# Optimization experiments

Hardware: AMD Instinct MI355X
Metric: run time of the kernel (lower is better)

## Reference

```python
import jax, jax.numpy as jnp
import numpy as np

MODEL_DIM = 1024
NUM_HEAD = 16
HEAD_DIM = MODEL_DIM // NUM_HEAD
B, S = 2, 2048


def setup_inputs() -> dict:
    key = jax.random.key(0)
    ks = jax.random.split(key, 13)
    s = 1.0 / np.sqrt(MODEL_DIM)
    inp = {
        "q": jax.random.normal(ks[0], (B, S, MODEL_DIM), jnp.float32),
        "k": jax.random.normal(ks[1], (B, S, MODEL_DIM), jnp.float32),
        "v": jax.random.normal(ks[2], (B, S, MODEL_DIM), jnp.float32),
        "mask": jax.random.randint(ks[3], (S, S), 0, 2, jnp.int32),
        "w_q": jax.random.normal(ks[4], (MODEL_DIM, MODEL_DIM), jnp.float32) * s,
        "b_q": jax.random.normal(ks[5], (MODEL_DIM,), jnp.float32) * s,
        "w_k": jax.random.normal(ks[6], (MODEL_DIM, MODEL_DIM), jnp.float32) * s,
        "b_k": jax.random.normal(ks[7], (MODEL_DIM,), jnp.float32) * s,
        "w_v": jax.random.normal(ks[8], (MODEL_DIM, MODEL_DIM), jnp.float32) * s,
        "b_v": jax.random.normal(ks[9], (MODEL_DIM,), jnp.float32) * s,
        "w_o": jax.random.normal(ks[10], (MODEL_DIM, MODEL_DIM), jnp.float32) * s,
        "b_o": jax.random.normal(ks[11], (MODEL_DIM,), jnp.float32) * s,
    }
    return inp


def reference(q, k, v, mask, w_q, b_q, w_k, b_k, w_v, b_v, w_o, b_o):
    batch, seq_len, dim = q.shape
    # Linear projections (weights stored as [d_in, d_out])
    Q = q @ w_q + b_q
    K = k @ w_k + b_k
    V = v @ w_v + b_v
    # [B, H, S, Dh]
    Q = Q.reshape(batch, seq_len, NUM_HEAD, HEAD_DIM).transpose(0, 2, 1, 3)
    K = K.reshape(batch, seq_len, NUM_HEAD, HEAD_DIM).transpose(0, 2, 1, 3)
    V = V.reshape(batch, seq_len, NUM_HEAD, HEAD_DIM).transpose(0, 2, 1, 3)
    scores = jnp.einsum("bhqd,bhkd->bhqk", Q, K) / jnp.sqrt(
        jnp.asarray(HEAD_DIM, Q.dtype)
    )
    scores = jnp.where(mask == 0, jnp.asarray(-1e9, scores.dtype), scores)
    attn = jax.nn.softmax(scores, axis=-1)
    out = jnp.einsum("bhqk,bhkd->bhqd", attn, V)
    out = out.transpose(0, 2, 1, 3).reshape(batch, seq_len, dim)
    return out @ w_o + b_o
```

## Files before the change

### kernel.cpp

```cpp
#include <hip/hip_runtime.h>
#include <stdint.h>

typedef __bf16 bf16;
typedef _Float16 f16;
typedef __attribute__((ext_vector_type(4))) __bf16 bf16x4;
typedef __attribute__((ext_vector_type(8))) __bf16 bf16x8;
typedef __attribute__((ext_vector_type(8))) _Float16 f16x8;
typedef __attribute__((ext_vector_type(4))) float f32x4;
typedef __attribute__((ext_vector_type(2))) float f32x2;
typedef __attribute__((ext_vector_type(2))) unsigned int u32x2;
typedef __attribute__((ext_vector_type(4))) unsigned int u32x4;

constexpr int S = 2048;
constexpr int D = 1024;
constexpr int H = 16;
constexpr int DH = 64;
constexpr int M = 4096;

constexpr float QSCALE = 0.18033688011112042f;

#if __has_builtin(__builtin_amdgcn_permlane32_swap) && \
    __has_builtin(__builtin_amdgcn_permlane16_swap)
#define REG_P 1
#define ATTN_SMEM 32768
#else
#define REG_P 0
#define ATTN_SMEM 49152
#endif

__device__ __forceinline__ void async16(void* lds, const void* g) {
  __builtin_amdgcn_global_load_lds(
      (const __attribute__((address_space(1))) void*)g,
      (__attribute__((address_space(3))) void*)lds, 16, 0, 0);
}

__global__ __launch_bounds__(256) void prep(
    const int* __restrict__ mask, uint64_t* __restrict__ MB,
    const float* __restrict__ q, const float* __restrict__ k,
    const float* __restrict__ v, bf16* __restrict__ qA, bf16* __restrict__ kA,
    bf16* __restrict__ vA, const float* __restrict__ Wq,
    const float* __restrict__ Wk, const float* __restrict__ Wv,
    const float* __restrict__ Wo, bf16* __restrict__ WTq,
    bf16* __restrict__ WTk, bf16* __restrict__ WTv, f16* __restrict__ WoT) {
  __shared__ float T[64 * 68];
  const int bid = blockIdx.x;
  const int tid = threadIdx.x;

  if (bid < 16384) {
    const int gid = bid * 4 + (tid >> 6);
    const int lane = tid & 63;
    const int kt = gid >> 11;
    const int qq = gid & (S - 1);
    int mv = mask[(size_t)qq * S + kt * 64 + lane];
    uint64_t bits = __ballot(mv != 0);
    if (lane == 0) MB[(size_t)kt * S + qq] = bits;
    return;
  }

  if (bid < 28672) {
    const int idx = bid - 16384;
    const int z = idx >> 12;
    const int x = idx & 4095;
    const float* src = (z == 0) ? q : (z == 1) ? k : v;
    bf16* dst = (z == 0) ? qA : (z == 1) ? kA : vA;
    const size_t i = ((size_t)x * 256 + tid) * 4;
    f32x4 xv = *(const f32x4*)(src + i);
    bf16x4 o;
#pragma unroll
    for (int j = 0; j < 4; j++) o[j] = (bf16)xv[j];
    *(bf16x4*)(dst + i) = o;
    return;
  }

  const int idx = bid - 28672;
  const int z = idx >> 8;
  const int xy = idx & 255;
  const int n0 = (xy >> 4) * 64, k0 = (xy & 15) * 64;
  const float* W = (z == 0) ? Wq : (z == 1) ? Wk : (z == 2) ? Wv : Wo;
  const int lr = tid >> 4, lc = (tid & 15) * 4;
#pragma unroll
  for (int r = 0; r < 4; r++) {
    f32x4 vv = *(const f32x4*)(W + (size_t)(k0 + r * 16 + lr) * 1024 + n0 + lc);
    *(f32x4*)&T[(r * 16 + lr) * 68 + lc] = vv;
  }
  __syncthreads();
  const int nn = tid >> 3, kc = (tid & 7) * 8;
#pragma unroll
  for (int p = 0; p < 2; p++) {
    int n = p * 32 + nn;
    if (z < 3) {
      bf16x8 h;
#pragma unroll
      for (int j = 0; j < 8; j++) h[j] = (bf16)T[(kc + j) * 68 + n];
      bf16* WT = (z == 0) ? WTq : (z == 1) ? WTk : WTv;
      *(bf16x8*)(WT + (size_t)(n0 + n) * 1024 + k0 + kc) = h;
    } else {
      f16x8 hf;
#pragma unroll
      for (int j = 0; j < 8; j++) hf[j] = (f16)T[(kc + j) * 68 + n];
      *(f16x8*)(WoT + (size_t)(n0 + n) * 1024 + k0 + kc) = hf;
    }
  }
}

__global__ __launch_bounds__(256) void gemm_qkv(
    const bf16* __restrict__ Aq, const bf16* __restrict__ Ak,
    const bf16* __restrict__ Av, const bf16* __restrict__ WTq,
    const bf16* __restrict__ WTk, const bf16* __restrict__ WTv,
    const float* __restrict__ bq, const float* __restrict__ bk,
    const float* __restrict__ bv, bf16* __restrict__ Qb,
    bf16* __restrict__ Kb, bf16* __restrict__ VT) {
  __shared__ char smem[34816];

  const int z = blockIdx.z;
  const bf16* A = (z == 0) ? Aq : (z == 1) ? Ak : Av;
  const bf16* WT = (z == 0) ? WTq : (z == 1) ? WTk : WTv;
  const float* bias = (z == 0) ? bq : (z == 1) ? bk : bv;
  const float oscale = (z == 0) ? QSCALE : 1.0f;

  const int tid = threadIdx.x;
  const int bn = blockIdx.x * 128;
  const int bm = blockIdx.y * 128;
  const int wv = tid >> 6;
  const int lane = tid & 63;
  const int quad = lane >> 4;
  const int lo = lane & 15;
  const int wm4 = (wv >> 1) * 4096;
  const int wn4 = (wv & 1) * 4096;

  f32x4 acc[4][4];
#pragma unroll
  for (int i = 0; i < 4; i++)
#pragma unroll
    for (int j = 0; j < 4; j++) acc[i][j] = {0.f, 0.f, 0.f, 0.f};

  const int pl = lane >> 3;
  const int uu = lane & 7;
  const int srow = pl * 2 + (uu & 1);
  const int sg = (uu >> 1) ^ (pl & 3);
  const int uread = (((quad ^ ((lo >> 1) & 3)) << 1) | (lo & 1)) * 16;
  const int aoff = (lo >> 1) * 128 + uread;

#define QSTAGE(kt_, buf_)                                                      \
  {                                                                            \
    _Pragma("unroll") for (int j = 0; j < 4; j++) {                            \
      int c = wv * 4 + j;               \
      if (c < 8) {                                                             \
        async16((buf_) + c * 1024,                                             \
                A + (size_t)(bm + c * 16 + srow) * 1024 + (kt_)*32 + sg * 8);  \
      } else {                                                                 \
        int cb = c - 8;                                                        \
        async16((buf_) + 8192 + cb * 1024,                                     \
                WT + (size_t)(bn + cb * 16 + srow) * 1024 + (kt_)*32 + sg * 8);\
      }                                                                        \
    }                                                                          \
  }

  QSTAGE(0, smem);

  for (int kt = 0; kt < 32; ++kt) {
    const char* cur = smem + (kt & 1) * 16384;
    __syncthreads();
    if (kt + 1 < 32) QSTAGE(kt + 1, smem + ((kt + 1) & 1) * 16384);

    bf16x8 af[4], bfr[4];
#pragma unroll
    for (int mi = 0; mi < 4; mi++)
      af[mi] = *(const bf16x8*)(cur + wm4 + mi * 1024 + aoff);
#pragma unroll
    for (int ni = 0; ni < 4; ni++)
      bfr[ni] = *(const bf16x8*)(cur + 8192 + wn4 + ni * 1024 + aoff);
#pragma unroll
    for (int mi = 0; mi < 4; mi++)
#pragma unroll
      for (int ni = 0; ni < 4; ni++)
        acc[mi][ni] = __builtin_amdgcn_mfma_f32_16x16x32_bf16(
            af[mi], bfr[ni], acc[mi][ni], 0, 0, 0);
  }
#undef QSTAGE

  const int b = bm >> 11;
  const int srow0 = bm & (S - 1);
  const int wm = (wv >> 1) * 64;
  const int wn = (wv & 1) * 64;

  if (z == 2) {
#pragma unroll
    for (int mi = 0; mi < 4; mi++)
#pragma unroll
      for (int ni = 0; ni < 4; ni++) {
        int col = bn + wn + ni * 16 + lo;
        int h = col >> 6, dh = col & 63;
        float bvv = bias[col];
        bf16x4 t;
#pragma unroll
        for (int r = 0; r < 4; r++) t[r] = (bf16)(acc[mi][ni][r] + bvv);
        int s0 = srow0 + wm + mi * 16 + quad * 4;
        *(bf16x4*)&VT[(((size_t)(b * H + h)) * DH + dh) * S + s0] = t;
      }
    return;
  }

  __syncthreads();
  bf16* T = (bf16*)smem;
#pragma unroll
  for (int mi = 0; mi < 4; mi++)
#pragma unroll
    for (int ni = 0; ni < 4; ni++) {
      int col = wn + ni * 16 + lo;
      float bvv = bias[bn + col];
#pragma unroll
      for (int r = 0; r < 4; r++) {
        int row = wm + mi * 16 + quad * 4 + r;
        T[row * 136 + col] = (bf16)((acc[mi][ni][r] + bvv) * oscale);
      }
    }
  __syncthreads();
  bf16* out = (z == 0) ? Qb : Kb;
  const int rr = tid >> 1;
  const int half = tid & 1;
  const int h = (bn >> 6) + half;
  bf16* gp = out + (((size_t)(b * H + h)) * S + srow0 + rr) * DH;
#pragma unroll
  for (int j = 0; j < 8; j++)
    *(bf16x8*)(gp + j * 8) = *(const bf16x8*)&T[rr * 136 + half * 64 + j * 8];
}

__global__ __launch_bounds__(256) void gemm_o(
    const f16* __restrict__ A, const f16* __restrict__ WT,
    const float* __restrict__ bias, float* __restrict__ out) {
  __shared__ char smem[24576];

  const int tid = threadIdx.x;
  const int bn = blockIdx.x * 128;
  const int bm = blockIdx.y * 64;
  const int wv = tid >> 6;
  const int lane = tid & 63;
  const int quad = lane >> 4;
  const int lo = lane & 15;
  const int wm = (wv >> 1) * 32;
  const int wn = (wv & 1) * 64;

  f32x4 acc[2][4];
#pragma unroll
  for (int i = 0; i < 2; i++)
#pragma unroll
    for (int j = 0; j < 4; j++) acc[i][j] = {0.f, 0.f, 0.f, 0.f};

  const int rloc = lane >> 3;
  const int gx = (lane & 7) ^ rloc;
  const int rx = (lo & 7);

  for (int kt = 0; kt < 16; ++kt) {
#pragma unroll
    for (int j = 0; j < 2; j++) {
      int ch = wv * 2 + j;
      async16(smem + ch * 1024,
              A + (size_t)(bm + ch * 8 + rloc) * 1024 + kt * 64 + gx * 8);
    }
#pragma unroll
    for (int j = 0; j < 4; j++) {
      int ch = wv * 4 + j;
      async16(smem + 8192 + ch * 1024,
              WT + (size_t)(bn + ch * 8 + rloc) * 1024 + kt * 64 + gx * 8);
    }
    __syncthreads();

#pragma unroll
    for (int ks = 0; ks < 2; ks++) {
      f16x8 af[2], bfr[4];
#pragma unroll
      for (int mi = 0; mi < 2; mi++)
        af[mi] = *(const f16x8*)(smem + (wm + mi * 16 + lo) * 128 +
                                 (((ks * 4 + quad) ^ rx) * 16));
#pragma unroll
      for (int ni = 0; ni < 4; ni++)
        bfr[ni] = *(const f16x8*)(smem + 8192 + (wn + ni * 16 + lo) * 128 +
                                  (((ks * 4 + quad) ^ rx) * 16));
#pragma unroll
      for (int mi = 0; mi < 2; mi++)
#pragma unroll
        for (int ni = 0; ni < 4; ni++)
          acc[mi][ni] = __builtin_amdgcn_mfma_f32_16x16x32_f16(
              af[mi], bfr[ni], acc[mi][ni], 0, 0, 0);
    }
    __syncthreads();
  }

#pragma unroll
  for (int mi = 0; mi < 2; mi++)
#pragma unroll
    for (int ni = 0; ni < 4; ni++) {
      int col = bn + wn + ni * 16 + lo;
      float bvv = bias[col];
#pragma unroll
      for (int r = 0; r < 4; r++) {
        int row = bm + wm + mi * 16 + quad * 4 + r;
        out[(size_t)row * 1024 + col] = acc[mi][ni][r] + bvv;
      }
    }
}

__global__ __launch_bounds__(512) void attn_kernel(
    const bf16* __restrict__ Qg, const bf16* __restrict__ Kg,
    const bf16* __restrict__ VTg, const uint64_t* __restrict__ MB,
    f16* __restrict__ AO) {
  __shared__ char smem[ATTN_SMEM];

  const int tid = threadIdx.x;
  const int wv = tid >> 6;
  const int lane = tid & 63;
  const int quad = lane >> 4;
  const int lo = lane & 15;

  const int lin = blockIdx.x;
  const int bh = (lin & 7) * 4 + ((lin >> 3) & 3);
  const int qt = lin >> 5;
  const int qbase = qt * 128 + wv * 16;
  const size_t base = (size_t)bh * S * DH;
#if !REG_P
  bf16* Pw = (bf16*)(smem + 32768 + wv * 2048);
  const int xm = (lo & 7) << 1;
#endif

  const int c0 = wv * 2;
  const int rloc = lane >> 3;
  const int gx = (lane & 7) ^ rloc;
  const int rx = lo & 7;

  bf16x8 qf[2];
  {
    const bf16* qp = Qg + base + (size_t)(qbase + lo) * DH + quad * 8;
    qf[0] = *(const bf16x8*)qp;
    qf[1] = *(const bf16x8*)(qp + 32);
  }

  f32x4 Oacc[4];
#pragma unroll
  for (int j = 0; j < 4; j++) Oacc[j] = {0.f, 0.f, 0.f, 0.f};
  f32x2 lp = {0.f, 0.f};

#define STAGE(kt_, buf_)                                                       \
  {                                                                            \
    _Pragma("unroll") for (int j = 0; j < 2; j++) {                            \
      int c = c0 + j;                                                          \
      if (c < 8) {                                                             \
        async16((buf_) + c * 1024,                                             \
                Kg + base + (size_t)((kt_)*64 + c * 8 + rloc) * 64 + gx * 8);  \
      } else {                                                                 \
        int cv = c - 8;                                                        \
        async16((buf_) + 8192 + cv * 1024,                                     \
                VTg + base + (size_t)(cv * 8 + rloc) * S + (kt_)*64 + gx * 8); \
      }                                                                        \
    }                                                                          \
  }

  STAGE(0, smem);
  uint64_t mcur = MB[(size_t)0 * S + qbase + lo];

  for (int kt = 0; kt < 32; ++kt) {
    const char* cur = smem + (kt & 1) * 16384;

    uint64_t m0 = mcur >> (quad * 4);
    uint32_t mw[2] = {(uint32_t)m0, (uint32_t)(m0 >> 32)};

    __syncthreads();
    if (kt + 1 < 32) {
      STAGE(kt + 1, smem + ((kt + 1) & 1) * 16384);
      mcur = MB[(size_t)(kt + 1) * S + qbase + lo];
    }

    const char* Kls = cur;
    const char* Vls = cur + 8192;

    f32x4 sacc[4];
#pragma unroll
    for (int mi = 0; mi < 4; mi++) sacc[mi] = {0.f, 0.f, 0.f, 0.f};
    __builtin_amdgcn_s_setprio(1);
#pragma unroll
    for (int mi = 0; mi < 4; mi++) {
      bf16x8 k0 = *(const bf16x8*)(Kls + (mi * 16 + lo) * 128 + ((quad ^ rx) * 16));
      bf16x8 k1 = *(const bf16x8*)(Kls + (mi * 16 + lo) * 128 + (((4 + quad) ^ rx) * 16));
      sacc[mi] = __builtin_amdgcn_mfma_f32_16x16x32_bf16(k0, qf[0], sacc[mi], 0, 0, 0);
      sacc[mi] = __builtin_amdgcn_mfma_f32_16x16x32_bf16(k1, qf[1], sacc[mi], 0, 0, 0);
    }
    __builtin_amdgcn_s_setprio(0);

    uint32_t u0[4], u1[4];
#pragma unroll
    for (int mi = 0; mi < 4; mi++) {
      bf16x4 t;
#pragma unroll
      for (int r = 0; r < 4; r++) {
        float p = __builtin_amdgcn_exp2f(sacc[mi][r]);
        int ext = __builtin_amdgcn_sbfe((int)mw[mi >> 1], ((mi & 1) << 4) + r, 1);
        p = __builtin_bit_cast(float, __builtin_bit_cast(int, p) & ext);
        lp[r & 1] += p;
        t[r] = (bf16)p;
      }
#if REG_P
      u32x2 w = __builtin_bit_cast(u32x2, t);
      u0[mi] = w[0];
      u1[mi] = w[1];
#else
      (void)u0;
      (void)u1;
      *(bf16x4*)&Pw[lo * 64 + (((mi * 4 + quad) ^ xm) * 4)] = t;
#endif
    }

    __builtin_amdgcn_s_setprio(1);
#pragma unroll
    for (int kk = 0; kk < 2; kk++) {
      bf16x8 pa;
#if REG_P
      uint32_t a0 = u0[kk * 2], b0 = u0[kk * 2 + 1];
      uint32_t a1 = u1[kk * 2], b1 = u1[kk * 2 + 1];
      u32x2 r0 = __builtin_amdgcn_permlane32_swap(a0, b0, false, false);
      r0 = __builtin_amdgcn_permlane16_swap(r0[0], r0[1], false, false);
      u32x2 r1 = __builtin_amdgcn_permlane32_swap(a1, b1, false, false);
      r1 = __builtin_amdgcn_permlane16_swap(r1[0], r1[1], false, false);
      u32x4 paw = {r0[0], r1[0], r0[1], r1[1]};
      pa = __builtin_bit_cast(bf16x8, paw);
#else
      int g16 = kk * 8 + quad * 2;
      pa = *(const bf16x8*)&Pw[lo * 64 + ((g16 ^ xm) * 4)];
#endif
#pragma unroll
      for (int ni = 0; ni < 4; ni++) {
        bf16x8 vb = *(const bf16x8*)(Vls + (ni * 16 + lo) * 128 +
                                     (((kk * 4 + quad) ^ rx) * 16));
        Oacc[ni] = __builtin_amdgcn_mfma_f32_16x16x32_bf16(pa, vb, Oacc[ni], 0, 0, 0);
      }
    }
    __builtin_amdgcn_s_setprio(0);
  }
#undef STAGE

  float lpart = lp[0] + lp[1];
  lpart += __shfl_xor(lpart, 16);
  lpart += __shfl_xor(lpart, 32);

  const int b = bh >> 4, h = bh & (H - 1);
#pragma unroll
  for (int r = 0; r < 4; r++) {
    float inv = 1.0f / __shfl(lpart, quad * 4 + r);
    int q = qbase + quad * 4 + r;
    size_t rowoff = (size_t)(b * S + q) * D + h * DH;
#pragma unroll
    for (int ni = 0; ni < 4; ni++)
      AO[rowoff + ni * 16 + lo] = (f16)(Oacc[ni][r] * inv);
  }
}

extern "C" void kernel_launch(void* const* d_in, const int* in_sizes, int n_in,
                              void* d_out, int out_size, void* d_ws,
                              size_t ws_size, hipStream_t stream) {
  const float* q = (const float*)d_in[0];
  const float* k = (const float*)d_in[1];
  const float* v = (const float*)d_in[2];
  const int* mask = (const int*)d_in[3];
  const float* w_q = (const float*)d_in[4];
  const float* b_q = (const float*)d_in[5];
  const float* w_k = (const float*)d_in[6];
  const float* b_k = (const float*)d_in[7];
  const float* w_v = (const float*)d_in[8];
  const float* b_v = (const float*)d_in[9];
  const float* w_o = (const float*)d_in[10];
  const float* b_o = (const float*)d_in[11];

  char* w = (char*)d_ws;
  const size_t MiB = 1ull << 20;
  bf16* Qb = (bf16*)w;
  bf16* Kb = (bf16*)(w + 8 * MiB);
  bf16* VT = (bf16*)(w + 16 * MiB);
  bf16* qA = (bf16*)(w + 24 * MiB);
  bf16* kA = (bf16*)(w + 32 * MiB);
  bf16* vA = (bf16*)(w + 40 * MiB);
  f16* AO = (f16*)(w + 24 * MiB);
  bf16* WTq = (bf16*)(w + 48 * MiB);
  bf16* WTk = (bf16*)(w + 50 * MiB);
  bf16* WTv = (bf16*)(w + 52 * MiB);
  f16* WoT = (f16*)(w + 54 * MiB);
  uint64_t* MBits = (uint64_t*)(w + 58 * MiB);

  prep<<<29696, 256, 0, stream>>>(mask, MBits, q, k, v, qA, kA, vA, w_q, w_k,
                                  w_v, w_o, WTq, WTk, WTv, WoT);
  gemm_qkv<<<dim3(8, 32, 3), 256, 0, stream>>>(qA, kA, vA, WTq, WTk, WTv, b_q,
                                               b_k, b_v, Qb, Kb, VT);
  attn_kernel<<<dim3(512), 512, 0, stream>>>(Qb, Kb, VT, MBits, AO);
  gemm_o<<<dim3(8, 64), 256, 0, stream>>>(AO, WoT, b_o, (float*)d_out);
}
```

Baseline: 245.8 us.

## Double-buffer output projection GEMM with smaller K tiles and new swizzle

```diff
diff --git a/kernel.cpp b/kernel.cpp
--- a/kernel.cpp
+++ b/kernel.cpp
@@ -238,55 +238,62 @@
   const int lane = tid & 63;
   const int quad = lane >> 4;
   const int lo = lane & 15;
+  const int wm2 = (wv >> 1) * 2048;
+  const int wn4 = (wv & 1) * 4096;
+
+  f32x4 acc[2][4];
+#pragma unroll
+  for (int i = 0; i < 2; i++)
+#pragma unroll
+    for (int j = 0; j < 4; j++) acc[i][j] = {0.f, 0.f, 0.f, 0.f};
+
+  const int pl = lane >> 3;
+  const int uu = lane & 7;
+  const int srow = pl * 2 + (uu & 1);
+  const int sg = (uu >> 1) ^ (pl & 3);
+  const int uread = (((quad ^ ((lo >> 1) & 3)) << 1) | (lo & 1)) * 16;
+  const int aoff = (lo >> 1) * 128 + uread;
+
+#define OSTAGE(kt_, buf_)                                                      \
+  {                                                                            \
+    _Pragma("unroll") for (int j = 0; j < 3; j++) {                            \
+      int c = wv * 3 + j;               \
+      if (c < 4) {                                                             \
+        async16((buf_) + c * 1024,                                             \
+                A + (size_t)(bm + c * 16 + srow) * 1024 + (kt_)*32 + sg * 8);  \
+      } else {                                                                 \
+        int cb = c - 4;                                                        \
+        async16((buf_) + 4096 + cb * 1024,                                     \
+                WT + (size_t)(bn + cb * 16 + srow) * 1024 + (kt_)*32 + sg * 8);\
+      }                                                                        \
+    }                                                                          \
+  }
+
+  OSTAGE(0, smem);
+
+  for (int kt = 0; kt < 32; ++kt) {
+    const char* cur = smem + (kt & 1) * 12288;
+    __syncthreads();
+    if (kt + 1 < 32) OSTAGE(kt + 1, smem + ((kt + 1) & 1) * 12288);
+
+    f16x8 af[2], bfr[4];
+#pragma unroll
+    for (int mi = 0; mi < 2; mi++)
+      af[mi] = *(const f16x8*)(cur + wm2 + mi * 1024 + aoff);
+#pragma unroll
+    for (int ni = 0; ni < 4; ni++)
+      bfr[ni] = *(const f16x8*)(cur + 4096 + wn4 + ni * 1024 + aoff);
+#pragma unroll
+    for (int mi = 0; mi < 2; mi++)
+#pragma unroll
+      for (int ni = 0; ni < 4; ni++)
+        acc[mi][ni] = __builtin_amdgcn_mfma_f32_16x16x32_f16(
+            af[mi], bfr[ni], acc[mi][ni], 0, 0, 0);
+  }
+#undef OSTAGE
+
   const int wm = (wv >> 1) * 32;
   const int wn = (wv & 1) * 64;
-
-  f32x4 acc[2][4];
-#pragma unroll
-  for (int i = 0; i < 2; i++)
-#pragma unroll
-    for (int j = 0; j < 4; j++) acc[i][j] = {0.f, 0.f, 0.f, 0.f};
-
-  const int rloc = lane >> 3;
-  const int gx = (lane & 7) ^ rloc;
-  const int rx = (lo & 7);
-
-  for (int kt = 0; kt < 16; ++kt) {
-#pragma unroll
-    for (int j = 0; j < 2; j++) {
-      int ch = wv * 2 + j;
-      async16(smem + ch * 1024,
-              A + (size_t)(bm + ch * 8 + rloc) * 1024 + kt * 64 + gx * 8);
-    }
-#pragma unroll
-    for (int j = 0; j < 4; j++) {
-      int ch = wv * 4 + j;
-      async16(smem + 8192 + ch * 1024,
-              WT + (size_t)(bn + ch * 8 + rloc) * 1024 + kt * 64 + gx * 8);
-    }
-    __syncthreads();
-
-#pragma unroll
-    for (int ks = 0; ks < 2; ks++) {
-      f16x8 af[2], bfr[4];
-#pragma unroll
-      for (int mi = 0; mi < 2; mi++)
-        af[mi] = *(const f16x8*)(smem + (wm + mi * 16 + lo) * 128 +
-                                 (((ks * 4 + quad) ^ rx) * 16));
-#pragma unroll
-      for (int ni = 0; ni < 4; ni++)
-        bfr[ni] = *(const f16x8*)(smem + 8192 + (wn + ni * 16 + lo) * 128 +
-                                  (((ks * 4 + quad) ^ rx) * 16));
-#pragma unroll
-      for (int mi = 0; mi < 2; mi++)
-#pragma unroll
-        for (int ni = 0; ni < 4; ni++)
-          acc[mi][ni] = __builtin_amdgcn_mfma_f32_16x16x32_f16(
-              af[mi], bfr[ni], acc[mi][ni], 0, 0, 0);
-    }
-    __syncthreads();
-  }
-
 #pragma unroll
   for (int mi = 0; mi < 2; mi++)
 #pragma unroll
```

Result: no change. 246.0 us (+0.1%).
